# Kernel tuning notes

Hardware: AMD Instinct MI355X
Metric: run time of the kernel (lower is better)

Reference implementation:

```python
import jax, jax.numpy as jnp
import numpy as np
from jax import lax

HEADS = 8
DIM_HEAD = 64
NUM_LANDMARKS = 256
PINV_ITERS = 6
CONV_PAD = 33 // 2  # 16


def moore_penrose_pinv(x, iters):
    # x: [..., m, m]
    abs_x = jnp.abs(x)
    col = abs_x.sum(-1).max()
    row = abs_x.sum(-2).max()
    z = jnp.swapaxes(x, -1, -2) / (col * row)
    I = jnp.eye(x.shape[-1], dtype=x.dtype)
    for _ in range(iters):
        xz = x @ z
        z = 0.25 * (z @ (13.0 * I - xz @ (15.0 * I - xz @ (7.0 * I - xz))))
    return z


def setup_inputs() -> dict:
    key = jax.random.key(0)
    k1, k2, k3, k4, k5 = jax.random.split(key, 5)
    b, n, dim = 4, 4096, 512
    inner = HEADS * DIM_HEAD
    return {
        "x": jax.random.normal(k1, (b, n, dim), jnp.float32),
        "w_qkv": jax.random.normal(k2, (dim, 3 * inner), jnp.float32) * 0.02,
        "w_out": jax.random.normal(k3, (inner, dim), jnp.float32) * 0.02,
        "b_out": jax.random.normal(k4, (dim,), jnp.float32) * 0.02,
        "res_kernel": jax.random.normal(k5, (HEADS, 1, 33, 1), jnp.float32) * 0.1,
    }


def reference(x, w_qkv, w_out, b_out, res_kernel):
    b, n, dim = x.shape
    h, dh, m = HEADS, DIM_HEAD, NUM_LANDMARKS
    scale = dh ** -0.5
    # n chosen as a multiple of m, so the pad branch is a no-op.
    l = n // m  # tokens per landmark group

    qkv = x @ w_qkv  # [b, n, 3*h*dh]
    q, k, v = jnp.split(qkv, 3, axis=-1)
    to_heads = lambda t: t.reshape(b, n, h, dh).transpose(0, 2, 1, 3)  # [b,h,n,dh]
    q, k, v = to_heads(q), to_heads(k), to_heads(v)
    q = q * scale

    # landmarks: mean over consecutive groups of l tokens
    q_l = q.reshape(b, h, m, l, dh).sum(3) / l  # [b,h,m,dh]
    k_l = k.reshape(b, h, m, l, dh).sum(3) / l

    attn1 = jax.nn.softmax(jnp.einsum("bhnd,bhmd->bhnm", q, k_l), axis=-1)  # [b,h,n,m]
    attn2 = jax.nn.softmax(jnp.einsum("bhid,bhjd->bhij", q_l, k_l), axis=-1)  # [b,h,m,m]
    attn3 = jax.nn.softmax(jnp.einsum("bhmd,bhnd->bhmn", q_l, k), axis=-1)  # [b,h,m,n]

    attn2_pinv = moore_penrose_pinv(attn2, PINV_ITERS)
    out = (attn1 @ attn2_pinv) @ (attn3 @ v)  # [b,h,n,dh]

    # depthwise residual conv over the sequence dim (Conv2d(h, h, (33,1), groups=h))
    res = lax.conv_general_dilated(
        v, res_kernel, window_strides=(1, 1),
        padding=((CONV_PAD, CONV_PAD), (0, 0)),
        dimension_numbers=("NCHW", "OIHW", "NCHW"),
        feature_group_count=h,
    )
    out = out + res

    out = out.transpose(0, 2, 1, 3).reshape(b, n, h * dh)
    out = out @ w_out + b_out
    return out
```

## Files before the change

kernel.cpp:

```cpp
#include <hip/hip_runtime.h>

#define Nq   4096
#define DHq  64
#define Mq   256
#define BHq  32

using bf16 = __bf16;
using bf16x8 = __bf16 __attribute__((ext_vector_type(8)));
using bf16x4 = __bf16 __attribute__((ext_vector_type(4)));
using f32x4 = float __attribute__((ext_vector_type(4)));

__device__ __forceinline__ f32x4 mfma16(bf16x8 a, bf16x8 b, f32x4 c) {
  return __builtin_amdgcn_mfma_f32_16x16x32_bf16(a, b, c, 0, 0, 0);
}
__device__ __forceinline__ unsigned short f2bu(float f) {
  bf16 b = (bf16)f;
  return __builtin_bit_cast(unsigned short, b);
}
__device__ __forceinline__ void split_store(bf16* h, bf16* l, long idx, float v) {
  bf16 hi = (bf16)v;
  h[idx] = hi;
  l[idx] = (bf16)(v - (float)hi);
}

template<int ROWS, int SRC>
__device__ __forceinline__ void stageA(const void* src, long ld, long row0, int k0,
                                       bf16* dst, int t) {
#pragma unroll
  for (int c = 0; c < ROWS / 64; ++c) {
    int idx = t + 256 * c;
    int r = idx >> 2;
    int kc = (idx & 3) << 3;
    bf16x8 val;
    if constexpr (SRC == 0) {
      val = *(const bf16x8*)((const bf16*)src + (row0 + r) * ld + k0 + kc);
    } else if constexpr (SRC == 1) {
      const float* s = (const float*)src + (row0 + r) * ld + k0 + kc;
      float4 a = *(const float4*)s;
      float4 b = *(const float4*)(s + 4);
      val[0]=(bf16)a.x; val[1]=(bf16)a.y; val[2]=(bf16)a.z; val[3]=(bf16)a.w;
      val[4]=(bf16)b.x; val[5]=(bf16)b.y; val[6]=(bf16)b.z; val[7]=(bf16)b.w;
    } else {
      long m = row0 + r;
      long bb = m >> 12, ii = m & 4095;
      int k = k0 + kc;
      long h = k >> 6, d = k & 63;
      val = *(const bf16x8*)((const bf16*)src + (((bb * 8 + h) * 4096 + ii) * 64 + d));
    }
    *(bf16x8*)(dst + r * 40 + kc) = val;
  }
}

template<int COLS, bool F32>
__device__ __forceinline__ void stageBN(const void* src, long ld, long n0, int k0,
                                        unsigned int* dst, int t) {
  int kp = t >> 4;
  int nb = (t & 15) << 2;
#pragma unroll
  for (int g = 0; g < COLS / 64; ++g) {
    int n = nb + (g << 6);
    unsigned int w0, w1, w2, w3;
    if constexpr (F32) {
      const float* s0 = (const float*)src + (long)(k0 + 2 * kp) * ld + n0 + n;
      const float* s1 = s0 + ld;
      float4 a = *(const float4*)s0;
      float4 b = *(const float4*)s1;
      w0 = f2bu(a.x) | ((unsigned)f2bu(b.x) << 16);
      w1 = f2bu(a.y) | ((unsigned)f2bu(b.y) << 16);
      w2 = f2bu(a.z) | ((unsigned)f2bu(b.z) << 16);
      w3 = f2bu(a.w) | ((unsigned)f2bu(b.w) << 16);
    } else {
      const unsigned short* s0 = (const unsigned short*)src + (long)(k0 + 2 * kp) * ld + n0 + n;
      const unsigned short* s1 = s0 + ld;
      ushort4 a = *(const ushort4*)s0;
      ushort4 b = *(const ushort4*)s1;
      w0 = a.x | ((unsigned)b.x << 16);
      w1 = a.y | ((unsigned)b.y << 16);
      w2 = a.z | ((unsigned)b.z << 16);
      w3 = a.w | ((unsigned)b.w << 16);
    }
    dst[(n + 0) * 20 + kp] = w0;
    dst[(n + 1) * 20 + kp] = w1;
    dst[(n + 2) * 20 + kp] = w2;
    dst[(n + 3) * 20 + kp] = w3;
  }
}

#define EQKV 0
#define EA2 1
#define EY 4
#define EG2 5
#define EG3 6
#define EG4 7
#define EWT 8
#define EBIAS 9

struct GP {
  const void* A; const void* Al;
  const void* B; const void* Bl;
  long ldA, ldB, sA, sB;
  int K;
  void* C0; void* C1; void* C2;
  long sC, ldC;
  const void* x0; const void* x1;
  const float* bias;
};

template<int BM, int BN, int WX, int ASRC, int BMODE, int SPLIT, int EPI, int SWZ>
__global__ __launch_bounds__(256, 2) void mgemm(GP p) {
  constexpr int WY = 4 / WX;
  constexpr int TM = BM / WY, TN = BN / WX;
  constexpr int IT = TM / 16, JT = TN / 16;
  constexpr int AB = (SPLIT ? 2 : 1) * BM * 80;
  constexpr int BB = (SPLIT ? 2 : 1) * BN * 80;
  __shared__ __align__(16) char Lbuf[AB + BB];
  bf16* AsL = (bf16*)Lbuf;
  unsigned int* BsL = (unsigned int*)(Lbuf + AB);
  int t = threadIdx.x;
  int wv = t >> 6, lane = t & 63;
  int wy = wv / WX, wx = wv % WX;
  int qd = lane >> 4, lm = lane & 15;
  long bz, m0, n0;
  if constexpr (SWZ == 1) {
    int b = blockIdx.x, xcd = b & 7, s = b >> 3;
    bz = 0; m0 = (long)(xcd * 16 + s / 12) * BM; n0 = (long)(s % 12) * BN;
  } else if constexpr (SWZ == 2) {
    int b = blockIdx.x, xcd = b & 7, s = b >> 3;
    bz = 0; m0 = (long)(xcd * 16 + (s >> 2)) * BM; n0 = (long)(s & 3) * BN;
  } else {
    bz = blockIdx.z; m0 = (long)blockIdx.y * BM; n0 = (long)blockIdx.x * BN;
  }

  const void* Ap; const void* Alp = nullptr;
  if constexpr (ASRC == 0) Ap = (const bf16*)p.A + bz * p.sA;
  else Ap = p.A;
  if constexpr (SPLIT) Alp = (const bf16*)p.Al + bz * p.sA;
  const void* Bp; const void* Blp = nullptr;
  if constexpr (BMODE == 2) Bp = p.B;
  else Bp = (const bf16*)p.B + bz * p.sB;
  if constexpr (SPLIT) Blp = (const bf16*)p.Bl + bz * p.sB;

  f32x4 acc[IT][JT];
#pragma unroll
  for (int i = 0; i < IT; ++i)
#pragma unroll
    for (int j = 0; j < JT; ++j) acc[i][j] = (f32x4)0.0f;

  for (int k0 = 0; k0 < p.K; k0 += 32) {
    stageA<BM, ASRC>(Ap, p.ldA, m0, k0, AsL, t);
    if constexpr (SPLIT) stageA<BM, 0>(Alp, p.ldA, m0, k0, AsL + BM * 40, t);
    if constexpr (BMODE == 0) {
      stageA<BN, 0>(Bp, p.ldB, n0, k0, (bf16*)BsL, t);
      if constexpr (SPLIT) stageA<BN, 0>(Blp, p.ldB, n0, k0, (bf16*)BsL + BN * 40, t);
    } else {
      stageBN<BN, BMODE == 2>(Bp, p.ldB, n0, k0, BsL, t);
      if constexpr (SPLIT) stageBN<BN, false>(Blp, p.ldB, n0, k0, BsL + BN * 20, t);
    }
    __syncthreads();
    bf16x8 af[IT], afl[IT];
#pragma unroll
    for (int i = 0; i < IT; ++i) {
      int m = wy * TM + i * 16 + lm;
      af[i] = *(const bf16x8*)(AsL + m * 40 + qd * 8);
      if constexpr (SPLIT) afl[i] = *(const bf16x8*)(AsL + BM * 40 + m * 40 + qd * 8);
    }
#pragma unroll
    for (int j = 0; j < JT; ++j) {
      int n = wx * TN + j * 16 + lm;
      bf16x8 bf, bfl;
      if constexpr (BMODE == 0) {
        bf = *(const bf16x8*)((const bf16*)BsL + n * 40 + qd * 8);
        if constexpr (SPLIT) bfl = *(const bf16x8*)((const bf16*)BsL + BN * 40 + n * 40 + qd * 8);
      } else {
        bf = *(const bf16x8*)((const bf16*)(BsL + n * 20 + qd * 4));
        if constexpr (SPLIT) bfl = *(const bf16x8*)((const bf16*)(BsL + BN * 20 + n * 20 + qd * 4));
      }
#pragma unroll
      for (int i = 0; i < IT; ++i) {
        acc[i][j] = mfma16(af[i], bf, acc[i][j]);
        if constexpr (SPLIT) {
          acc[i][j] = mfma16(af[i], bfl, acc[i][j]);
          acc[i][j] = mfma16(afl[i], bf, acc[i][j]);
        }
      }
    }
    __syncthreads();
  }

  if constexpr (EPI == EA2) {
#pragma unroll
    for (int r = 0; r < 4; ++r) {
      long row = m0 + wy * TM + qd * 4 + r;
      float e[JT];
      float s = 0.f;
#pragma unroll
      for (int j = 0; j < JT; ++j) { e[j] = __expf(acc[0][j][r]); s += e[j]; }
      s += __shfl_xor(s, 1); s += __shfl_xor(s, 2);
      s += __shfl_xor(s, 4); s += __shfl_xor(s, 8);
      float inv = 1.0f / s;
#pragma unroll
      for (int j = 0; j < JT; ++j) {
        long col = n0 + j * 16 + lm;
        split_store((bf16*)p.C0, (bf16*)p.C1, bz * p.sC + row * p.ldC + col, e[j] * inv);
      }
    }
  } else {
#pragma unroll
    for (int i = 0; i < IT; ++i)
#pragma unroll
      for (int j = 0; j < JT; ++j)
#pragma unroll
        for (int r = 0; r < 4; ++r) {
          long row = m0 + wy * TM + i * 16 + qd * 4 + r;
          long col = n0 + wx * TN + j * 16 + lm;
          float v = acc[i][j][r];
          if constexpr (EPI == EQKV) {
            int part = (int)(col >> 9);
            long h = (col >> 6) & 7, d = col & 63;
            long bb = row >> 12, ii = row & 4095;
            float scv = part == 0 ? 0.125f : 1.0f;
            bf16* dst = part == 0 ? (bf16*)p.C0 : (part == 1 ? (bf16*)p.C1 : (bf16*)p.C2);
            dst[((bb * 8 + h) * 4096 + ii) * 64 + d] = (bf16)(v * scv);
          } else if constexpr (EPI == EY) {
            split_store((bf16*)p.C0, (bf16*)p.C1, bz * 65536 + row * 256 + col, v);
          } else if constexpr (EPI == EG2) {
            long ix = bz * 65536 + row * 256 + col;
            float y = (float)((const bf16*)p.x0)[ix] + (float)((const bf16*)p.x1)[ix];
            float val = (row == col ? 15.0f : 0.0f) - 7.0f * y + v;
            split_store((bf16*)p.C0, (bf16*)p.C1, ix, val);
          } else if constexpr (EPI == EG3) {
            float val = (row == col ? 13.0f : 0.0f) - v;
            split_store((bf16*)p.C0, (bf16*)p.C1, bz * 65536 + row * 256 + col, val);
          } else if constexpr (EPI == EG4) {
            split_store((bf16*)p.C0, (bf16*)p.C1, bz * 65536 + row * 256 + col, 0.25f * v);
          } else if constexpr (EPI == EWT) {
            ((bf16*)p.C0)[bz * 16384 + col * 256 + row] = (bf16)v;
          } else if constexpr (EPI == EBIAS) {
            ((float*)p.C0)[row * 512 + col] = v + p.bias[col];
          }
        }
  }
}


#define SBW 132

__device__ __forceinline__ void stageBS(const bf16* src, long n0, int k0,
                                        unsigned int* dst, int t) {
  int kp = t >> 4, nb = (t & 15) << 2;
  const unsigned short* s0 = (const unsigned short*)src + (long)(k0 + 2 * kp) * 256 + n0 + nb;
  const unsigned short* s1 = s0 + 256;
  ushort4 a = *(const ushort4*)s0;
  ushort4 b = *(const ushort4*)s1;
  int wb = (k0 >> 1) + kp;
  dst[(nb + 0) * SBW + wb] = a.x | ((unsigned)b.x << 16);
  dst[(nb + 1) * SBW + wb] = a.y | ((unsigned)b.y << 16);
  dst[(nb + 2) * SBW + wb] = a.z | ((unsigned)b.z << 16);
  dst[(nb + 3) * SBW + wb] = a.w | ((unsigned)b.w << 16);
}

template<int SPLIT>
__device__ __forceinline__ void sgemm(const bf16* Ah, const bf16* Al,
                                      const unsigned int* Bs, const unsigned int* Bsl,
                                      int w, int lane, f32x4 acc[2][4]) {
  int qd = lane >> 4, lm = lane & 15;
#pragma unroll
  for (int i = 0; i < 2; ++i)
#pragma unroll
    for (int j = 0; j < 4; ++j) acc[i][j] = (f32x4)0.0f;
#pragma unroll 2
  for (int k0 = 0; k0 < 256; k0 += 32) {
    bf16x8 af[2], afl[2];
#pragma unroll
    for (int i = 0; i < 2; ++i) {
      long m = w * 32 + i * 16 + lm;
      af[i] = *(const bf16x8*)(Ah + m * 256 + k0 + qd * 8);
      if constexpr (SPLIT) afl[i] = *(const bf16x8*)(Al + m * 256 + k0 + qd * 8);
    }
#pragma unroll
    for (int j = 0; j < 4; ++j) {
      bf16x8 bv = *(const bf16x8*)((const bf16*)(Bs + (j * 16 + lm) * SBW + (k0 >> 1) + qd * 4));
      bf16x8 bl;
      if constexpr (SPLIT)
        bl = *(const bf16x8*)((const bf16*)(Bsl + (j * 16 + lm) * SBW + (k0 >> 1) + qd * 4));
#pragma unroll
      for (int i = 0; i < 2; ++i) {
        acc[i][j] = mfma16(af[i], bv, acc[i][j]);
        if constexpr (SPLIT) {
          acc[i][j] = mfma16(af[i], bl, acc[i][j]);
          acc[i][j] = mfma16(afl[i], bv, acc[i][j]);
        }
      }
    }
  }
}

template<int SPLIT>
__global__ __launch_bounds__(512) void k_nsy(const bf16* __restrict__ A2h,
                                             const bf16* __restrict__ A2l,
                                             const bf16* __restrict__ zh,
                                             const bf16* __restrict__ zl,
                                             bf16* __restrict__ yh, bf16* __restrict__ yl) {
  __shared__ __align__(16) unsigned int Bs[2][64 * SBW];
  int b = blockIdx.x, t = threadIdx.x;
  long bh = b >> 2, js = (long)(b & 3) * 64;
  const bf16* Ah = A2h + bh * 65536;
  const bf16* Al = A2l + bh * 65536;
  const bf16* Bh = zh + bh * 65536;
  const bf16* Bl = zl + bh * 65536;
  if (t < 256) {
#pragma unroll
    for (int k0 = 0; k0 < 256; k0 += 32) {
      stageBS(Bh, js, k0, Bs[0], t);
      if constexpr (SPLIT) stageBS(Bl, js, k0, Bs[1], t);
    }
  }
  __syncthreads();
  int w = t >> 6, lane = t & 63;
  f32x4 acc[2][4];
  sgemm<SPLIT>(Ah, Al, Bs[0], Bs[1], w, lane, acc);
  int qd = lane >> 4, lm = lane & 15;
  bf16* yhb = yh + bh * 65536;
  bf16* ylb = yl + bh * 65536;
#pragma unroll
  for (int i = 0; i < 2; ++i)
#pragma unroll
    for (int j = 0; j < 4; ++j)
#pragma unroll
      for (int r = 0; r < 4; ++r) {
        long row = w * 32 + i * 16 + qd * 4 + r;
        long col = js + j * 16 + lm;
        split_store(yhb, ylb, row * 256 + col, acc[i][j][r]);
      }
}

template<int SPLIT>
__global__ __launch_bounds__(512) void k_ns3(const bf16* __restrict__ yh_,
                                             const bf16* __restrict__ yl_,
                                             const bf16* __restrict__ zh,
                                             const bf16* __restrict__ zl,
                                             bf16* __restrict__ znh, bf16* __restrict__ znl) {
  __shared__ __align__(16) unsigned int S0[2][64 * SBW];
  __shared__ __align__(16) unsigned int S1[2][64 * SBW];
  int b = blockIdx.x, t = threadIdx.x;
  long bh = b >> 2, js = (long)(b & 3) * 64;
  const bf16* yh = yh_ + bh * 65536;
  const bf16* yl = yl_ + bh * 65536;
  const bf16* zch = zh + bh * 65536;
  const bf16* zcl = zl + bh * 65536;
  if (t < 256) {
#pragma unroll
    for (int k0 = 0; k0 < 256; k0 += 32) {
      stageBS(yh, js, k0, S0[0], t);
      if constexpr (SPLIT) stageBS(yl, js, k0, S0[1], t);
    }
  }
  __syncthreads();
  int w = t >> 6, lane = t & 63, qd = lane >> 4, lm = lane & 15;
  f32x4 acc[2][4];

  sgemm<SPLIT>(yh, yl, S0[0], S0[1], w, lane, acc);
#pragma unroll
  for (int i = 0; i < 2; ++i)
#pragma unroll
    for (int j = 0; j < 4; ++j) {
      int R0 = w * 32 + i * 16 + qd * 4;
      int col = j * 16 + lm;
      float v[4];
#pragma unroll
      for (int r = 0; r < 4; ++r) {
        long row = R0 + r;
        long ix = row * 256 + js + col;
        float yv = (float)yh[ix] + (float)yl[ix];
        v[r] = ((row == js + col) ? 15.0f : 0.0f) - 7.0f * yv + acc[i][j][r];
      }
      unsigned int* Wp = S1[0] + col * SBW + (R0 >> 1);
      Wp[0] = f2bu(v[0]) | ((unsigned)f2bu(v[1]) << 16);
      Wp[1] = f2bu(v[2]) | ((unsigned)f2bu(v[3]) << 16);
      if constexpr (SPLIT) {
        unsigned int* Wq = S1[1] + col * SBW + (R0 >> 1);
        Wq[0] = f2bu(v[0] - (float)(bf16)v[0]) | ((unsigned)f2bu(v[1] - (float)(bf16)v[1]) << 16);
        Wq[1] = f2bu(v[2] - (float)(bf16)v[2]) | ((unsigned)f2bu(v[3] - (float)(bf16)v[3]) << 16);
      }
    }
  __syncthreads();

  sgemm<SPLIT>(yh, yl, S1[0], S1[1], w, lane, acc);
#pragma unroll
  for (int i = 0; i < 2; ++i)
#pragma unroll
    for (int j = 0; j < 4; ++j) {
      int R0 = w * 32 + i * 16 + qd * 4;
      int col = j * 16 + lm;
      float v[4];
#pragma unroll
      for (int r = 0; r < 4; ++r)
        v[r] = (((long)(R0 + r) == js + col) ? 13.0f : 0.0f) - acc[i][j][r];
      unsigned int* Wp = S0[0] + col * SBW + (R0 >> 1);
      Wp[0] = f2bu(v[0]) | ((unsigned)f2bu(v[1]) << 16);
      Wp[1] = f2bu(v[2]) | ((unsigned)f2bu(v[3]) << 16);
      if constexpr (SPLIT) {
        unsigned int* Wq = S0[1] + col * SBW + (R0 >> 1);
        Wq[0] = f2bu(v[0] - (float)(bf16)v[0]) | ((unsigned)f2bu(v[1] - (float)(bf16)v[1]) << 16);
        Wq[1] = f2bu(v[2] - (float)(bf16)v[2]) | ((unsigned)f2bu(v[3] - (float)(bf16)v[3]) << 16);
      }
    }
  __syncthreads();

  sgemm<SPLIT>(zch, zcl, S0[0], S0[1], w, lane, acc);
  bf16* zoh = znh + bh * 65536;
  bf16* zol = znl + bh * 65536;
#pragma unroll
  for (int i = 0; i < 2; ++i)
#pragma unroll
    for (int j = 0; j < 4; ++j)
#pragma unroll
      for (int r = 0; r < 4; ++r) {
        long row = w * 32 + i * 16 + qd * 4 + r;
        long col = js + j * 16 + lm;
        split_store(zoh, zol, row * 256 + col, 0.25f * acc[i][j][r]);
      }
}

__global__ __launch_bounds__(256, 2) void k_a3v(const bf16* __restrict__ qlh,
                                                const bf16* __restrict__ kb,
                                                const bf16* __restrict__ vb,
                                                float* __restrict__ a3vf,
                                                float* __restrict__ rs3) {
  __shared__ __align__(16) char L[38400];
  bf16* qlS = (bf16*)L;
  bf16* kS  = (bf16*)(L + 9216);
  bf16* PA  = (bf16*)(L + 18432);
  unsigned int* vB0 = (unsigned int*)(L + 27648);
  unsigned int* vB1 = (unsigned int*)(L + 32768);
  float* rsL = (float*)(L + 37888);
  int b = blockIdx.x, t = threadIdx.x;
  int xcd = b & 7, s = b >> 3;
  int strip = xcd * 16 + (s >> 2);
  int qt = s & 3;
  long bz = strip >> 2;
  int kt = strip & 3;
  int wv = t >> 6, lane = t & 63, qd = lane >> 4, lm = lane & 15;
  int wy = wv >> 1, wx = wv & 1;
  const bf16* qlp = qlh + bz * 16384 + qt * 64 * 64;
#pragma unroll
  for (int c = 0; c < 2; ++c) {
    int idx = t + 256 * c;
    int r = idx >> 3, dc = (idx & 7) * 8;
    *(bf16x8*)(qlS + r * 72 + dc) = *(const bf16x8*)(qlp + r * 64 + dc);
  }
  const bf16* kb_ = kb + bz * 262144 + (long)kt * 65536;
  const bf16* vb_ = vb + bz * 262144 + (long)kt * 65536;
  f32x4 accO[2][2];
  float rsum[2][4];
#pragma unroll
  for (int i = 0; i < 2; ++i) {
#pragma unroll
    for (int j = 0; j < 2; ++j) accO[i][j] = (f32x4)0.0f;
#pragma unroll
    for (int r = 0; r < 4; ++r) rsum[i][r] = 0.f;
  }
  for (int tt = 0; tt < 16; ++tt) {
    __syncthreads();
    const bf16* ks_ = kb_ + tt * 4096;
#pragma unroll
    for (int c = 0; c < 2; ++c) {
      int idx = t + 256 * c;
      int r = idx >> 3, dc = (idx & 7) * 8;
      *(bf16x8*)(kS + r * 72 + dc) = *(const bf16x8*)(ks_ + r * 64 + dc);
    }
    const bf16* vs_ = vb_ + tt * 4096;
    stageBN<64, false>(vs_, 64, 0, 0, vB0, t);
    stageBN<64, false>(vs_, 64, 0, 32, vB1, t);
    __syncthreads();
    f32x4 s2[2][2];
#pragma unroll
    for (int i = 0; i < 2; ++i)
#pragma unroll
      for (int j = 0; j < 2; ++j) s2[i][j] = (f32x4)0.0f;
#pragma unroll
    for (int ks = 0; ks < 2; ++ks) {
      bf16x8 af[2], bfv[2];
#pragma unroll
      for (int i = 0; i < 2; ++i)
        af[i] = *(const bf16x8*)(qlS + (wy * 32 + i * 16 + lm) * 72 + ks * 32 + qd * 8);
#pragma unroll
      for (int j = 0; j < 2; ++j)
        bfv[j] = *(const bf16x8*)(kS + (wx * 32 + j * 16 + lm) * 72 + ks * 32 + qd * 8);
#pragma unroll
      for (int i = 0; i < 2; ++i)
#pragma unroll
        for (int j = 0; j < 2; ++j) s2[i][j] = mfma16(af[i], bfv[j], s2[i][j]);
    }
#pragma unroll
    for (int i = 0; i < 2; ++i)
#pragma unroll
      for (int r = 0; r < 4; ++r) {
        float e0 = __expf(s2[i][0][r]);
        float e1 = __expf(s2[i][1][r]);
        int row = wy * 32 + i * 16 + qd * 4 + r;
        PA[row * 72 + wx * 32 + 0 * 16 + lm] = (bf16)e0;
        PA[row * 72 + wx * 32 + 1 * 16 + lm] = (bf16)e1;
        float cs = e0 + e1;
        cs += __shfl_xor(cs, 1); cs += __shfl_xor(cs, 2);
        cs += __shfl_xor(cs, 4); cs += __shfl_xor(cs, 8);
        rsum[i][r] += cs;
      }
    __syncthreads();
#pragma unroll
    for (int ks = 0; ks < 2; ++ks) {
      unsigned int* vB = ks ? vB1 : vB0;
      bf16x8 af[2], bfv[2];
#pragma unroll
      for (int i = 0; i < 2; ++i)
        af[i] = *(const bf16x8*)(PA + (wy * 32 + i * 16 + lm) * 72 + ks * 32 + qd * 8);
#pragma unroll
      for (int j = 0; j < 2; ++j)
        bfv[j] = *(const bf16x8*)((const bf16*)(vB + (wx * 32 + j * 16 + lm) * 20) + qd * 8);
#pragma unroll
      for (int i = 0; i < 2; ++i)
#pragma unroll
        for (int j = 0; j < 2; ++j) accO[i][j] = mfma16(af[i], bfv[j], accO[i][j]);
    }
  }
  if (lm == 0) {
#pragma unroll
    for (int i = 0; i < 2; ++i)
#pragma unroll
      for (int r = 0; r < 4; ++r)
        rsL[(wy * 32 + i * 16 + qd * 4 + r) * 2 + wx] = rsum[i][r];
  }
  __syncthreads();
  if (t < 64) atomicAdd(&rs3[bz * 256 + qt * 64 + t], rsL[t * 2] + rsL[t * 2 + 1]);
#pragma unroll
  for (int i = 0; i < 2; ++i)
#pragma unroll
    for (int j = 0; j < 2; ++j)
#pragma unroll
      for (int r = 0; r < 4; ++r) {
        long row = bz * 256 + qt * 64 + wy * 32 + i * 16 + qd * 4 + r;
        long col = wx * 32 + j * 16 + lm;
        atomicAdd(&a3vf[row * 64 + col], accO[i][j][r]);
      }
}

__global__ void k_a3vnorm(const float* __restrict__ a3vf, const float* __restrict__ rs3,
                          bf16* __restrict__ a3vh, bf16* __restrict__ a3vl) {
  long e0 = ((long)blockIdx.x * 256 + threadIdx.x) * 4;
  float4 vv = *(const float4*)&a3vf[e0];
  float inv = 1.0f / rs3[e0 >> 6];
  split_store(a3vh, a3vl, e0 + 0, vv.x * inv);
  split_store(a3vh, a3vl, e0 + 1, vv.y * inv);
  split_store(a3vh, a3vl, e0 + 2, vv.z * inv);
  split_store(a3vh, a3vl, e0 + 3, vv.w * inv);
}

__global__ void k_zero(float* a3vf, float* rs3, unsigned int* sc) {
  long i = (long)blockIdx.x * 256 + threadIdx.x;
  a3vf[i] = 0.f;
  if (i < 8192) rs3[i] = 0.f;
  if (i == 0) sc[0] = 0u;
}

__global__ void k_landmarks(const bf16* q, const bf16* k, bf16* qlh, bf16* qll,
                            bf16* klh, bf16* kll) {
  int bm = blockIdx.x;
  int bh = bm >> 8, mi = bm & 255;
  int d = threadIdx.x;
  const bf16* qp = q + ((long)bh * 4096 + mi * 16) * 64 + d;
  const bf16* kp = k + ((long)bh * 4096 + mi * 16) * 64 + d;
  float sq = 0.f, sk = 0.f;
#pragma unroll
  for (int tt = 0; tt < 16; ++tt) { sq += (float)qp[tt * 64]; sk += (float)kp[tt * 64]; }
  sq *= 0.0625f; sk *= 0.0625f;
  long o = (long)bh * 16384 + mi * 64 + d;
  split_store(qlh, qll, o, sq);
  split_store(klh, kll, o, sk);
}

__global__ __launch_bounds__(256) void k_colsum(const bf16* A2h, const bf16* A2l,
                                                unsigned int* sc) {
  int bh = blockIdx.x, j = threadIdx.x;
  const bf16* ph = A2h + (long)bh * 65536 + j;
  const bf16* pl = A2l + (long)bh * 65536 + j;
  float s = 0.f;
  for (int i = 0; i < 256; ++i) s += (float)ph[i * 256] + (float)pl[i * 256];
  __shared__ float red[256];
  red[j] = s; __syncthreads();
  for (int o = 128; o > 0; o >>= 1) {
    if (j < o) red[j] = fmaxf(red[j], red[j + o]);
    __syncthreads();
  }
  if (j == 0) atomicMax(sc, __float_as_uint(red[0]));
}

__global__ __launch_bounds__(256) void k_zinit(const bf16* A2h, const bf16* A2l,
                                               const unsigned int* sc, bf16* zh, bf16* zl) {
  __shared__ float T[64][65];
  int bh = blockIdx.z, ti = blockIdx.y, tj = blockIdx.x;
  int t = threadIdx.x;
  int c = t & 63, r0 = t >> 6;
  long base = (long)bh * 65536;
  float inv = 1.0f / __uint_as_float(sc[0]);
#pragma unroll
  for (int rr = 0; rr < 16; ++rr) {
    int r = r0 * 16 + rr;
    long idx = base + (long)(ti * 64 + r) * 256 + tj * 64 + c;
    T[r][c] = (float)A2h[idx] + (float)A2l[idx];
  }
  __syncthreads();
#pragma unroll
  for (int rr = 0; rr < 16; ++rr) {
    int jl = r0 * 16 + rr;
    float v = T[c][jl] * inv;
    long o = base + (long)(tj * 64 + jl) * 256 + ti * 64 + c;
    split_store(zh, zl, o, v);
  }
}

__global__ __launch_bounds__(256, 2) void k_attn1w(const bf16* qb, const bf16* klb,
                                                   const bf16* Wt, bf16* oh) {
  __shared__ __align__(16) char L[38912];
  bf16* Aq = (bf16*)L;
  bf16* Bkl = (bf16*)(L + 5120);
  bf16* Pl = (bf16*)L;
  bf16* Bw = (bf16*)(L + 33792);
  int t = threadIdx.x, wv = t >> 6, lane = t & 63;
  int qd = lane >> 4, lm = lane & 15;
  long bz = blockIdx.z;
  long m0 = (long)blockIdx.x * 64;
  const bf16* qA = qb + bz * (4096L * 64);
  const bf16* klA = klb + bz * (256L * 64);
  const bf16* WtA = Wt + bz * 16384;

  f32x4 a1[16];
#pragma unroll
  for (int j = 0; j < 16; ++j) a1[j] = (f32x4)0.0f;
  for (int k0 = 0; k0 < 64; k0 += 32) {
    stageA<64, 0>(qA, 64, m0, k0, Aq, t);
    stageA<256, 0>(klA, 64, 0, k0, Bkl, t);
    __syncthreads();
    bf16x8 af = *(const bf16x8*)(Aq + (wv * 16 + lm) * 40 + qd * 8);
#pragma unroll
    for (int j = 0; j < 16; ++j) {
      bf16x8 bf = *(const bf16x8*)(Bkl + (j * 16 + lm) * 40 + qd * 8);
      a1[j] = mfma16(af, bf, a1[j]);
    }
    __syncthreads();
  }
  float rs[4];
#pragma unroll
  for (int r = 0; r < 4; ++r) {
    int rowl = wv * 16 + qd * 4 + r;
    float ev[16];
    float s = 0.f;
#pragma unroll
    for (int j = 0; j < 16; ++j) { ev[j] = __expf(a1[j][r]); s += ev[j]; }
    s += __shfl_xor(s, 1); s += __shfl_xor(s, 2);
    s += __shfl_xor(s, 4); s += __shfl_xor(s, 8);
    rs[r] = s;
#pragma unroll
    for (int j = 0; j < 16; ++j) {
      float other = __shfl_xor(ev[j], 1);
      if ((lm & 1) == 0) {
        unsigned int w = f2bu(ev[j]) | ((unsigned)f2bu(other) << 16);
        *(unsigned int*)(Pl + rowl * 264 + j * 16 + lm) = w;
      }
    }
  }
  f32x4 a2[4];
#pragma unroll
  for (int j = 0; j < 4; ++j) a2[j] = (f32x4)0.0f;
  for (int k0 = 0; k0 < 256; k0 += 32) {
    stageA<64, 0>(WtA, 256, 0, k0, Bw, t);
    __syncthreads();
    bf16x8 af = *(const bf16x8*)(Pl + (wv * 16 + lm) * 264 + k0 + qd * 8);
#pragma unroll
    for (int j = 0; j < 4; ++j) {
      bf16x8 bf = *(const bf16x8*)(Bw + (j * 16 + lm) * 40 + qd * 8);
      a2[j] = mfma16(af, bf, a2[j]);
    }
    __syncthreads();
  }
#pragma unroll
  for (int j = 0; j < 4; ++j)
#pragma unroll
    for (int r = 0; r < 4; ++r) {
      long grow = m0 + wv * 16 + qd * 4 + r;
      long col = j * 16 + lm;
      oh[(bz * 4096 + grow) * 64 + col] = (bf16)(a2[j][r] / rs[r]);
    }
}

__global__ __launch_bounds__(256) void k_conv2(const bf16* __restrict__ v,
                                               const float* __restrict__ kern,
                                               bf16* __restrict__ oh) {
  __shared__ __align__(16) bf16 Vs[96 * 72];
  int bx = blockIdx.x;
  int bh = bx >> 6;
  int i0 = (bx & 63) * 64;
  int t = threadIdx.x;
  const bf16* vsrc = v + (long)bh * 262144;
#pragma unroll
  for (int c = 0; c < 3; ++c) {
    int idx = t + 256 * c;
    int r = idx >> 3, dc = (idx & 7) * 8;
    int grow = i0 + r - 16;
    bf16x8 val = (bf16x8)(bf16)0.0f;
    if (grow >= 0 && grow < 4096) val = *(const bf16x8*)(vsrc + (long)grow * 64 + dc);
    *(bf16x8*)(Vs + r * 72 + dc) = val;
  }
  __syncthreads();
  int dg = t & 15, rg = t >> 4;
  const float* kc = kern + (bh & 7) * 33;
  float acc[4][4] = {};
#pragma unroll
  for (int rr = 0; rr < 36; ++rr) {
    bf16x4 xv = *(const bf16x4*)(Vs + (rg * 4 + rr) * 72 + dg * 4);
    float x0 = (float)xv[0], x1 = (float)xv[1], x2 = (float)xv[2], x3 = (float)xv[3];
#pragma unroll
    for (int r = 0; r < 4; ++r) {
      int u = rr - r;
      if (u >= 0 && u < 33) {
        float kw = kc[u];
        acc[r][0] = fmaf(kw, x0, acc[r][0]);
        acc[r][1] = fmaf(kw, x1, acc[r][1]);
        acc[r][2] = fmaf(kw, x2, acc[r][2]);
        acc[r][3] = fmaf(kw, x3, acc[r][3]);
      }
    }
  }
  long base = ((long)bh * 4096 + i0 + rg * 4) * 64 + dg * 4;
#pragma unroll
  for (int r = 0; r < 4; ++r) {
    bf16x4 o = *(const bf16x4*)(oh + base + r * 64);
    bf16x4 w;
#pragma unroll
    for (int c = 0; c < 4; ++c) w[c] = (bf16)(acc[r][c] + (float)o[c]);
    *(bf16x4*)(oh + base + r * 64) = w;
  }
}

extern "C" void kernel_launch(void* const* d_in, const int* in_sizes, int n_in,
                              void* d_out, int out_size, void* d_ws, size_t ws_size,
                              hipStream_t stream) {
  const float* x     = (const float*)d_in[0];
  const float* w_qkv = (const float*)d_in[1];
  const float* w_out = (const float*)d_in[2];
  const float* b_out = (const float*)d_in[3];
  const float* res_k = (const float*)d_in[4];

  char* w = (char*)d_ws;
  bf16* qb  = (bf16*)(w);
  bf16* kb  = (bf16*)(w + 16777216);
  bf16* vb  = (bf16*)(w + 33554432);
  bf16* qlh = (bf16*)(w + 50331648);
  bf16* qll = (bf16*)(w + 51380224);
  bf16* klh = (bf16*)(w + 52428800);
  bf16* kll = (bf16*)(w + 53477376);
  bf16* A2h = (bf16*)(w + 54525952);
  bf16* A2l = (bf16*)(w + 58720256);
  bf16* zAh = (bf16*)(w + 62914560);
  bf16* zAl = (bf16*)(w + 67108864);
  bf16* zBh = (bf16*)(w + 71303168);
  bf16* zBl = (bf16*)(w + 75497472);
  bf16* yh  = (bf16*)(w + 79691776);
  bf16* yl  = (bf16*)(w + 83886080);
  bf16* bbh = (bf16*)(w + 88080384);
  bf16* bbl = (bf16*)(w + 92274688);
  bf16* cch = (bf16*)(w + 96468992);
  bf16* ccl = (bf16*)(w + 100663296);
  bf16* oh  = (bf16*)(w + 104857600);
  float* a3vf = (float*)(w + 121634816);
  bf16* a3vh = (bf16*)(w + 123731968);
  bf16* a3vl = (bf16*)(w + 124780544);
  bf16* Wt   = (bf16*)(w + 125829120);
  float* rs3 = (float*)(w + 126877696);
  unsigned int* sc  = (unsigned int*)(w + 126910464);

  k_zero<<<2048, 256, 0, stream>>>(a3vf, rs3, sc);

  GP p{};
  p.A = x; p.ldA = 512; p.B = w_qkv; p.ldB = 1536; p.K = 512;
  p.C0 = qb; p.C1 = kb; p.C2 = vb;
  mgemm<128, 128, 2, 1, 2, 0, EQKV, 1><<<1536, 256, 0, stream>>>(p);

  k_landmarks<<<8192, 64, 0, stream>>>(qb, kb, qlh, qll, klh, kll);

  p = GP{};
  p.A = qlh; p.Al = qll; p.ldA = 64; p.sA = 16384;
  p.B = klh; p.Bl = kll; p.ldB = 64; p.sB = 16384; p.K = 64;
  p.C0 = A2h; p.C1 = A2l; p.sC = 65536; p.ldC = 256;
  mgemm<64, 256, 1, 0, 0, 1, EA2, 0><<<dim3(1, 4, 32), 256, 0, stream>>>(p);

  k_colsum<<<32, 256, 0, stream>>>(A2h, A2l, sc);
  k_zinit<<<dim3(4, 4, 32), 256, 0, stream>>>(A2h, A2l, sc, zAh, zAl);

  k_a3v<<<512, 256, 0, stream>>>(qlh, kb, vb, a3vf, rs3);
  k_a3vnorm<<<512, 256, 0, stream>>>(a3vf, rs3, a3vh, a3vl);

  bf16 *zch = zAh, *zcl = zAl, *znh = zBh, *znl = zBl;
  for (int it = 0; it < 6; ++it) {
    if (it < 4) {
      k_nsy<0><<<128, 512, 0, stream>>>(A2h, A2l, zch, zcl, yh, yl);
      k_ns3<0><<<128, 512, 0, stream>>>(yh, yl, zch, zcl, znh, znl);
    } else {
      k_nsy<1><<<128, 512, 0, stream>>>(A2h, A2l, zch, zcl, yh, yl);
      k_ns3<1><<<128, 512, 0, stream>>>(yh, yl, zch, zcl, znh, znl);
    }
    bf16* tmp;
    tmp = zch; zch = znh; znh = tmp;
    tmp = zcl; zcl = znl; znl = tmp;
  }

  p = GP{};
  p.A = zch; p.Al = zcl; p.ldA = 256; p.sA = 65536;
  p.B = a3vh; p.Bl = a3vl; p.ldB = 64; p.sB = 16384; p.K = 256;
  p.C0 = Wt;
  mgemm<64, 64, 2, 0, 1, 1, EWT, 0><<<dim3(1, 4, 32), 256, 0, stream>>>(p);

  k_attn1w<<<dim3(64, 1, 32), 256, 0, stream>>>(qb, klh, Wt, oh);

  k_conv2<<<2048, 256, 0, stream>>>(vb, res_k, oh);

  p = GP{};
  p.A = oh; p.B = w_out; p.ldB = 512; p.K = 512;
  p.C0 = d_out; p.bias = b_out;
  mgemm<128, 128, 2, 3, 2, 0, EBIAS, 2><<<512, 256, 0, stream>>>(p);
}
```

Measured before the change: 513.2 us.

## Use direct global-to-LDS loads for QKV and output projection GEMMs

Adds a dedicated ggemm kernel for the two large projection GEMMs. It stages A and B tiles with global_load_lds, which writes straight from global memory into LDS without going through registers. To make that possible, x is pre-cast to bf16 and both weight matrices are transposed to bf16 K-contiguous layout in separate small kernels. The goal is to remove the register round-trip and the on-the-fly fp32 conversion and transposed B staging from the GEMM inner loop. The cost is three extra launches and extra passes over x and the weights, plus unused mgemm code paths removed. The LDS tiles are unpadded, so bank conflicts on the fragment reads are possible.

```diff
diff --git a/kernel.cpp b/kernel.cpp
--- a/kernel.cpp
+++ b/kernel.cpp
@@ -21,6 +21,12 @@
   bf16 hi = (bf16)v;
   h[idx] = hi;
   l[idx] = (bf16)(v - (float)hi);
+}
+
+typedef const __attribute__((address_space(1))) void* gas_t;
+typedef __attribute__((address_space(3))) void* las_t;
+__device__ __forceinline__ void glds16(const bf16* g, bf16* l) {
+  __builtin_amdgcn_global_load_lds((gas_t)g, (las_t)l, 16, 0, 0);
 }
 
 template<int ROWS, int SRC>
@@ -34,18 +40,12 @@
     bf16x8 val;
     if constexpr (SRC == 0) {
       val = *(const bf16x8*)((const bf16*)src + (row0 + r) * ld + k0 + kc);
-    } else if constexpr (SRC == 1) {
+    } else {
       const float* s = (const float*)src + (row0 + r) * ld + k0 + kc;
       float4 a = *(const float4*)s;
       float4 b = *(const float4*)(s + 4);
       val[0]=(bf16)a.x; val[1]=(bf16)a.y; val[2]=(bf16)a.z; val[3]=(bf16)a.w;
       val[4]=(bf16)b.x; val[5]=(bf16)b.y; val[6]=(bf16)b.z; val[7]=(bf16)b.w;
-    } else {
-      long m = row0 + r;
-      long bb = m >> 12, ii = m & 4095;
-      int k = k0 + kc;
-      long h = k >> 6, d = k & 63;
-      val = *(const bf16x8*)((const bf16*)src + (((bb * 8 + h) * 4096 + ii) * 64 + d));
     }
     *(bf16x8*)(dst + r * 40 + kc) = val;
   }
@@ -89,9 +89,6 @@
 #define EQKV 0
 #define EA2 1
 #define EY 4
-#define EG2 5
-#define EG3 6
-#define EG4 7
 #define EWT 8
 #define EBIAS 9
 
@@ -120,24 +117,13 @@
   int wv = t >> 6, lane = t & 63;
   int wy = wv / WX, wx = wv % WX;
   int qd = lane >> 4, lm = lane & 15;
-  long bz, m0, n0;
-  if constexpr (SWZ == 1) {
-    int b = blockIdx.x, xcd = b & 7, s = b >> 3;
-    bz = 0; m0 = (long)(xcd * 16 + s / 12) * BM; n0 = (long)(s % 12) * BN;
-  } else if constexpr (SWZ == 2) {
-    int b = blockIdx.x, xcd = b & 7, s = b >> 3;
-    bz = 0; m0 = (long)(xcd * 16 + (s >> 2)) * BM; n0 = (long)(s & 3) * BN;
-  } else {
-    bz = blockIdx.z; m0 = (long)blockIdx.y * BM; n0 = (long)blockIdx.x * BN;
-  }
-
-  const void* Ap; const void* Alp = nullptr;
-  if constexpr (ASRC == 0) Ap = (const bf16*)p.A + bz * p.sA;
-  else Ap = p.A;
+  long bz = blockIdx.z, m0 = (long)blockIdx.y * BM, n0 = (long)blockIdx.x * BN;
+
+  const void* Ap = (const bf16*)p.A + bz * p.sA;
+  const void* Alp = nullptr;
   if constexpr (SPLIT) Alp = (const bf16*)p.Al + bz * p.sA;
-  const void* Bp; const void* Blp = nullptr;
-  if constexpr (BMODE == 2) Bp = p.B;
-  else Bp = (const bf16*)p.B + bz * p.sB;
+  const void* Bp = (const bf16*)p.B + bz * p.sB;
+  const void* Blp = nullptr;
   if constexpr (SPLIT) Blp = (const bf16*)p.Bl + bz * p.sB;
 
   f32x4 acc[IT][JT];
@@ -153,7 +139,7 @@
       stageA<BN, 0>(Bp, p.ldB, n0, k0, (bf16*)BsL, t);
       if constexpr (SPLIT) stageA<BN, 0>(Blp, p.ldB, n0, k0, (bf16*)BsL + BN * 40, t);
     } else {
-      stageBN<BN, BMODE == 2>(Bp, p.ldB, n0, k0, BsL, t);
+      stageBN<BN, false>(Bp, p.ldB, n0, k0, BsL, t);
       if constexpr (SPLIT) stageBN<BN, false>(Blp, p.ldB, n0, k0, BsL + BN * 20, t);
     }
     __syncthreads();
@@ -214,34 +200,124 @@
           long row = m0 + wy * TM + i * 16 + qd * 4 + r;
           long col = n0 + wx * TN + j * 16 + lm;
           float v = acc[i][j][r];
-          if constexpr (EPI == EQKV) {
-            int part = (int)(col >> 9);
-            long h = (col >> 6) & 7, d = col & 63;
-            long bb = row >> 12, ii = row & 4095;
-            float scv = part == 0 ? 0.125f : 1.0f;
-            bf16* dst = part == 0 ? (bf16*)p.C0 : (part == 1 ? (bf16*)p.C1 : (bf16*)p.C2);
-            dst[((bb * 8 + h) * 4096 + ii) * 64 + d] = (bf16)(v * scv);
-          } else if constexpr (EPI == EY) {
+          if constexpr (EPI == EY) {
             split_store((bf16*)p.C0, (bf16*)p.C1, bz * 65536 + row * 256 + col, v);
-          } else if constexpr (EPI == EG2) {
-            long ix = bz * 65536 + row * 256 + col;
-            float y = (float)((const bf16*)p.x0)[ix] + (float)((const bf16*)p.x1)[ix];
-            float val = (row == col ? 15.0f : 0.0f) - 7.0f * y + v;
-            split_store((bf16*)p.C0, (bf16*)p.C1, ix, val);
-          } else if constexpr (EPI == EG3) {
-            float val = (row == col ? 13.0f : 0.0f) - v;
-            split_store((bf16*)p.C0, (bf16*)p.C1, bz * 65536 + row * 256 + col, val);
-          } else if constexpr (EPI == EG4) {
-            split_store((bf16*)p.C0, (bf16*)p.C1, bz * 65536 + row * 256 + col, 0.25f * v);
           } else if constexpr (EPI == EWT) {
             ((bf16*)p.C0)[bz * 16384 + col * 256 + row] = (bf16)v;
-          } else if constexpr (EPI == EBIAS) {
-            ((float*)p.C0)[row * 512 + col] = v + p.bias[col];
           }
         }
   }
 }
 
+template<int ASRC, int EPI, int SWZ>
+__global__ __launch_bounds__(256, 3) void ggemm(GP p) {
+  __shared__ __align__(64) bf16 AsL[128 * 32];
+  __shared__ __align__(64) bf16 BsL[128 * 32];
+  int t = threadIdx.x, wv = t >> 6, lane = t & 63;
+  int wy = wv >> 1, wx = wv & 1;
+  int qd = lane >> 4, lm = lane & 15;
+  long m0, n0;
+  if constexpr (SWZ == 1) {
+    int b = blockIdx.x, xcd = b & 7, s = b >> 3;
+    m0 = (long)(xcd * 16 + s / 12) * 128; n0 = (long)(s % 12) * 128;
+  } else {
+    int b = blockIdx.x, xcd = b & 7, s = b >> 3;
+    m0 = (long)(xcd * 16 + (s >> 2)) * 128; n0 = (long)(s & 3) * 128;
+  }
+  const bf16* A = (const bf16*)p.A;
+  const bf16* B = (const bf16*)p.B;
+
+  f32x4 acc[4][4];
+#pragma unroll
+  for (int i = 0; i < 4; ++i)
+#pragma unroll
+    for (int j = 0; j < 4; ++j) acc[i][j] = (f32x4)0.0f;
+
+  int rsub = lane >> 2;
+  int kc = (lane & 3) << 3;
+  for (int k0 = 0; k0 < p.K; k0 += 32) {
+#pragma unroll
+    for (int e = 0; e < 2; ++e) {
+      int br = wv * 32 + e * 16;
+      long rA = m0 + br + rsub;
+      const bf16* gA;
+      if constexpr (ASRC == 0) {
+        gA = A + rA * p.ldA + k0 + kc;
+      } else {
+        long bb = rA >> 12, ii = rA & 4095;
+        int k = k0 + kc;
+        long h = k >> 6, d = k & 63;
+        gA = A + (((bb * 8 + h) * 4096 + ii) * 64 + d);
+      }
+      glds16(gA, AsL + br * 32);
+      const bf16* gB = B + (n0 + br + rsub) * p.ldB + k0 + kc;
+      glds16(gB, BsL + br * 32);
+    }
+    __syncthreads();
+    bf16x8 af[4];
+#pragma unroll
+    for (int i = 0; i < 4; ++i)
+      af[i] = *(const bf16x8*)(AsL + (wy * 64 + i * 16 + lm) * 32 + qd * 8);
+#pragma unroll
+    for (int j = 0; j < 4; ++j) {
+      bf16x8 bv = *(const bf16x8*)(BsL + (wx * 64 + j * 16 + lm) * 32 + qd * 8);
+#pragma unroll
+      for (int i = 0; i < 4; ++i) acc[i][j] = mfma16(af[i], bv, acc[i][j]);
+    }
+    __syncthreads();
+  }
+
+#pragma unroll
+  for (int i = 0; i < 4; ++i)
+#pragma unroll
+    for (int j = 0; j < 4; ++j)
+#pragma unroll
+      for (int r = 0; r < 4; ++r) {
+        long row = m0 + wy * 64 + i * 16 + qd * 4 + r;
+        long col = n0 + wx * 64 + j * 16 + lm;
+        float v = acc[i][j][r];
+        if constexpr (EPI == EQKV) {
+          int part = (int)(col >> 9);
+          long h = (col >> 6) & 7, d = col & 63;
+          long bb = row >> 12, ii = row & 4095;
+          float scv = part == 0 ? 0.125f : 1.0f;
+          bf16* dst = part == 0 ? (bf16*)p.C0 : (part == 1 ? (bf16*)p.C1 : (bf16*)p.C2);
+          dst[((bb * 8 + h) * 4096 + ii) * 64 + d] = (bf16)(v * scv);
+        } else {
+          ((float*)p.C0)[row * 512 + col] = v + p.bias[col];
+        }
+      }
+}
+
+__global__ __launch_bounds__(256) void k_xcast(const float* __restrict__ x,
+                                               bf16* __restrict__ xb) {
+  long i = ((long)blockIdx.x * 256 + threadIdx.x) * 8;
+  float4 a = *(const float4*)(x + i);
+  float4 b = *(const float4*)(x + i + 4);
+  bf16x8 v;
+  v[0]=(bf16)a.x; v[1]=(bf16)a.y; v[2]=(bf16)a.z; v[3]=(bf16)a.w;
+  v[4]=(bf16)b.x; v[5]=(bf16)b.y; v[6]=(bf16)b.z; v[7]=(bf16)b.w;
+  *(bf16x8*)(xb + i) = v;
+}
+
+__global__ __launch_bounds__(256) void k_wtrans(const float* __restrict__ src,
+                                                bf16* __restrict__ dst, int N) {
+  __shared__ float T[64][65];
+  int tj = blockIdx.x, ti = blockIdx.y;
+  int t = threadIdx.x;
+  int c = t & 63, r0 = t >> 6;
+#pragma unroll
+  for (int rr = 0; rr < 16; ++rr) {
+    int r = r0 * 16 + rr;
+    T[r][c] = src[(long)(ti * 64 + r) * N + tj * 64 + c];
+  }
+  __syncthreads();
+#pragma unroll
+  for (int rr = 0; rr < 16; ++rr) {
+    int n = r0 * 16 + rr;
+    dst[(long)(tj * 64 + n) * 512 + ti * 64 + c] = (bf16)T[c][n];
+  }
+}
 
 #define SBW 132
 
@@ -766,11 +842,10 @@
   bf16* zBl = (bf16*)(w + 75497472);
   bf16* yh  = (bf16*)(w + 79691776);
   bf16* yl  = (bf16*)(w + 83886080);
-  bf16* bbh = (bf16*)(w + 88080384);
-  bf16* bbl = (bf16*)(w + 92274688);
-  bf16* cch = (bf16*)(w + 96468992);
-  bf16* ccl = (bf16*)(w + 100663296);
+  bf16* wqt = (bf16*)(w + 88080384);
+  bf16* wot = (bf16*)(w + 89653248);
   bf16* oh  = (bf16*)(w + 104857600);
+  bf16* xb  = (bf16*)(w + 104857600);
   float* a3vf = (float*)(w + 121634816);
   bf16* a3vh = (bf16*)(w + 123731968);
   bf16* a3vl = (bf16*)(w + 124780544);
@@ -780,10 +855,14 @@
 
   k_zero<<<2048, 256, 0, stream>>>(a3vf, rs3, sc);
 
+  k_xcast<<<4096, 256, 0, stream>>>(x, xb);
+  k_wtrans<<<dim3(24, 8), 256, 0, stream>>>(w_qkv, wqt, 1536);
+  k_wtrans<<<dim3(8, 8), 256, 0, stream>>>(w_out, wot, 512);
+
   GP p{};
-  p.A = x; p.ldA = 512; p.B = w_qkv; p.ldB = 1536; p.K = 512;
+  p.A = xb; p.ldA = 512; p.B = wqt; p.ldB = 512; p.K = 512;
   p.C0 = qb; p.C1 = kb; p.C2 = vb;
-  mgemm<128, 128, 2, 1, 2, 0, EQKV, 1><<<1536, 256, 0, stream>>>(p);
+  ggemm<0, EQKV, 1><<<1536, 256, 0, stream>>>(p);
 
   k_landmarks<<<8192, 64, 0, stream>>>(qb, kb, qlh, qll, klh, kll);
 
@@ -824,7 +903,7 @@
   k_conv2<<<2048, 256, 0, stream>>>(vb, res_k, oh);
 
   p = GP{};
-  p.A = oh; p.B = w_out; p.ldB = 512; p.K = 512;
+  p.A = oh; p.ldA = 64; p.B = wot; p.ldB = 512; p.K = 512;
   p.C0 = d_out; p.bias = b_out;
-  mgemm<128, 128, 2, 3, 2, 0, EBIAS, 2><<<512, 256, 0, stream>>>(p);
-}
+  ggemm<3, EBIAS, 2><<<512, 256, 0, stream>>>(p);
+}
```

Result: no change. 509.4 us (-0.7%).
